# Optimization experiments

Measured on AMD Instinct MI355X. Metric: run time of the kernel, lower is better.

Reference implementation:

```python
import jax, jax.numpy as jnp
import numpy as np

EMB = 256  # embedding_dim


def setup_inputs() -> dict:
    key = jax.random.key(0)
    k1, k2, k3 = jax.random.split(key, 3)
    B, P, N, D = 32, 4, 1024, EMB
    x = jax.random.normal(k1, (B, P, N, D), dtype=jnp.float32)
    W_qkv = jax.random.normal(k2, (D, 1 + 2 * D), dtype=jnp.float32) * (1.0 / np.sqrt(D))
    b_qkv = jnp.zeros((1 + 2 * D,), dtype=jnp.float32)
    W_o = jax.random.normal(k3, (D, D), dtype=jnp.float32) * (1.0 / np.sqrt(D))
    b_o = jnp.zeros((D,), dtype=jnp.float32)
    return {"x": x, "W_qkv": W_qkv, "b_qkv": b_qkv, "W_o": W_o, "b_o": b_o}


def reference(x, W_qkv, b_qkv, W_o, b_o):
    # x: [B, P, N, D]
    D = W_o.shape[0]
    qkv = jnp.einsum('bpnd,de->bpne', x, W_qkv) + b_qkv  # [B,P,N,1+2D]
    q = qkv[..., :1]                 # [B,P,N,1]
    k = qkv[..., 1:1 + D]            # [B,P,N,D]
    v = jax.nn.relu(qkv[..., 1 + D:])  # [B,P,N,D]
    # softmax over the patch axis N (axis=2)
    context_scores = jax.nn.softmax(q, axis=2)  # [B,P,N,1]
    # dropout layers operate in inference mode here (identity)
    context_vector = jnp.sum(k * context_scores, axis=2, keepdims=True)  # [B,P,1,D]
    updated_values = v * context_vector  # broadcast multiply, [B,P,N,D]
    final = jnp.einsum('bpnd,de->bpne', updated_values, W_o) + b_o  # [B,P,N,D]
    return final
```

## Files before the change

### kernel.cpp

```cpp
#include <hip/hip_runtime.h>


typedef float  floatx4 __attribute__((ext_vector_type(4)));
typedef __bf16 bf16x8  __attribute__((ext_vector_type(8)));
typedef unsigned short u16;
typedef u16 u16x8 __attribute__((ext_vector_type(8)));

#define NGRP 128

__device__ __forceinline__ float bf2f(u16 u) {
    union { unsigned int i; float f; } c; c.i = ((unsigned int)u) << 16; return c.f;
}
__device__ __forceinline__ u16 f2bf(float f) {
    union { __bf16 h; u16 u; } c; c.h = (__bf16)f; return c.u;
}
__device__ __forceinline__ floatx4 mfma16(bf16x8 a, bf16x8 b, floatx4 c) {
    return __builtin_amdgcn_mfma_f32_16x16x32_bf16(a, b, c, 0, 0, 0);
}

__global__ __launch_bounds__(256) void k_prep(
    const float* __restrict__ Wqkv, const float* __restrict__ Wo,
    u16* __restrict__ Wvp, u16* __restrict__ Wop,
    float* __restrict__ wqp, float* __restrict__ y, float* __restrict__ Sg)
{
    const int i = blockIdx.x * 256 + threadIdx.x;
    const int j = i & 7, lane = (i >> 3) & 63, kk = (i >> 9) & 7, ct = i >> 12;
    const int k = kk * 32 + (lane >> 4) * 8 + j;
    Wvp[i] = f2bf(Wqkv[k * 513 + (257 + ct * 16 + (lane & 15))]);
    Wop[i] = f2bf(Wo[k * 256 + (ct * 16 + (lane & 15))]);
    if (i < 256) wqp[i] = Wqkv[i * 513];
    if (i < NGRP * 256) y[i] = 0.f;
    if (i < NGRP) Sg[i] = 0.f;
}

__global__ __launch_bounds__(256) void k_sum(
    const float* __restrict__ x, const float* __restrict__ wqp,
    const float* __restrict__ bqkv,
    float* __restrict__ y, float* __restrict__ Sg)
{
    const int tid = threadIdx.x;
    const int m0 = blockIdx.x * 64;
    const int g  = blockIdx.x >> 4;
    __shared__ float e_s[64];

    {
        const int r = tid >> 2, s = tid & 3;
        const float* xp = x + (size_t)(m0 + r) * 256 + s * 4;
        const float* wp = wqp + s * 4;
        float q = 0.f;
#pragma unroll
        for (int j = 0; j < 16; j++) {
            floatx4 xv = *(const floatx4*)(xp + j * 16);
            floatx4 wv = *(const floatx4*)(wp + j * 16);
            q += xv[0] * wv[0] + xv[1] * wv[1] + xv[2] * wv[2] + xv[3] * wv[3];
        }
        q += __shfl_xor(q, 1, 64);
        q += __shfl_xor(q, 2, 64);
        if (s == 0) e_s[r] = __expf(q + bqkv[0]);
    }
    __syncthreads();

    if (tid < 64) {
        float e = e_s[tid];
#pragma unroll
        for (int s = 32; s > 0; s >>= 1) e += __shfl_xor(e, s, 64);
        if (tid == 0) atomicAdd(Sg + g, e);
    }

    {
        float acc = 0.f;
        const float* xp = x + (size_t)m0 * 256 + tid;
#pragma unroll 8
        for (int r = 0; r < 64; r++) acc += e_s[r] * xp[r * 256];
        atomicAdd(y + g * 256 + tid, acc);
    }
}

__global__ __launch_bounds__(256) void k_cv(
    const float* __restrict__ Wqkv, const float* __restrict__ bqkv,
    const float* __restrict__ y, const float* __restrict__ Sg,
    float* __restrict__ cv)
{
    const int g = blockIdx.x, d = threadIdx.x;
    __shared__ float ys[256];
    ys[d] = y[g * 256 + d] * (1.0f / Sg[g]);
    __syncthreads();
    float acc = bqkv[1 + d];
    const float* wp = Wqkv + 1 + d;
#pragma unroll 4
    for (int t = 0; t < 256; t++) acc += ys[t] * wp[t * 513];
    cv[g * 256 + d] = acc;
}

__global__ __launch_bounds__(512, 4) void k_vo(
    const float* __restrict__ x, const u16* __restrict__ Wvp,
    const u16* __restrict__ Wop, const float* __restrict__ cv,
    const float* __restrict__ bqkv, const float* __restrict__ bo,
    float* __restrict__ out)
{
    const int tid = threadIdx.x;
    const int w = tid >> 6, lane = tid & 63, quad = lane >> 4, n16 = lane & 15;
    const int m0 = blockIdx.x * 64;
    const int g  = blockIdx.x >> 4;

    __shared__ u16 As[64 * 256];
    __shared__ float cvs[256];

    if (tid < 256) cvs[tid] = cv[g * 256 + tid];

#pragma unroll
    for (int it = 0; it < 4; it++) {
        const int c = it * 512 + tid;
        const int row = c >> 5, col = c & 31;
        const float* xp = x + (size_t)(m0 + row) * 256 + col * 8;
        floatx4 u0 = *(const floatx4*)xp;
        floatx4 u1 = *(const floatx4*)(xp + 4);
        u16x8 o;
        o[0] = f2bf(u0[0]); o[1] = f2bf(u0[1]); o[2] = f2bf(u0[2]); o[3] = f2bf(u0[3]);
        o[4] = f2bf(u1[0]); o[5] = f2bf(u1[1]); o[6] = f2bf(u1[2]); o[7] = f2bf(u1[3]);
        *(u16x8*)(As + row * 256 + ((col ^ (row & 15)) * 8)) = o;
    }
    __syncthreads();

    floatx4 acc[2][4];
#pragma unroll
    for (int i = 0; i < 2; i++)
#pragma unroll
        for (int rt = 0; rt < 4; rt++) acc[i][rt] = (floatx4){0.f, 0.f, 0.f, 0.f};

#pragma unroll
    for (int kk = 0; kk < 8; kk++) {
        bf16x8 a[4];
#pragma unroll
        for (int rt = 0; rt < 4; rt++) {
            const int row = rt * 16 + n16;
            a[rt] = __builtin_bit_cast(bf16x8,
                *(const u16x8*)(As + row * 256 + (((kk * 4 + quad) ^ n16) * 8)));
        }
#pragma unroll
        for (int i = 0; i < 2; i++) {
            const int ct = w + 8 * i;
            bf16x8 b = __builtin_bit_cast(bf16x8,
                *(const u16x8*)(Wvp + (size_t)((ct * 8 + kk) * 64 + lane) * 8));
#pragma unroll
            for (int rt = 0; rt < 4; rt++) acc[i][rt] = mfma16(a[rt], b, acc[i][rt]);
        }
    }
    __syncthreads();

#pragma unroll
    for (int i = 0; i < 2; i++) {
        const int col = (w + 8 * i) * 16 + n16;
        const float bias = bqkv[257 + col];
        const float scale = cvs[col];
        const int cc = col >> 3, co = col & 7;
#pragma unroll
        for (int rt = 0; rt < 4; rt++) {
#pragma unroll
            for (int r = 0; r < 4; r++) {
                const int row = rt * 16 + quad * 4 + r;
                const float vv = fmaxf(acc[i][rt][r] + bias, 0.f) * scale;
                As[row * 256 + ((cc ^ (row & 15)) * 8) + co] = f2bf(vv);
            }
        }
    }
    __syncthreads();

    floatx4 acc2[2][4];
#pragma unroll
    for (int i = 0; i < 2; i++)
#pragma unroll
        for (int rt = 0; rt < 4; rt++) acc2[i][rt] = (floatx4){0.f, 0.f, 0.f, 0.f};

#pragma unroll
    for (int kk = 0; kk < 8; kk++) {
        bf16x8 a[4];
#pragma unroll
        for (int rt = 0; rt < 4; rt++) {
            const int row = rt * 16 + n16;
            a[rt] = __builtin_bit_cast(bf16x8,
                *(const u16x8*)(As + row * 256 + (((kk * 4 + quad) ^ n16) * 8)));
        }
#pragma unroll
        for (int i = 0; i < 2; i++) {
            const int ct = w + 8 * i;
            bf16x8 b = __builtin_bit_cast(bf16x8,
                *(const u16x8*)(Wop + (size_t)((ct * 8 + kk) * 64 + lane) * 8));
#pragma unroll
            for (int rt = 0; rt < 4; rt++) acc2[i][rt] = mfma16(a[rt], b, acc2[i][rt]);
        }
    }

#pragma unroll
    for (int i = 0; i < 2; i++) {
        const int col = (w + 8 * i) * 16 + n16;
        const float bias = bo[col];
#pragma unroll
        for (int rt = 0; rt < 4; rt++) {
            const int rowb = m0 + rt * 16 + quad * 4;
#pragma unroll
            for (int r = 0; r < 4; r++)
                out[(size_t)(rowb + r) * 256 + col] = acc2[i][rt][r] + bias;
        }
    }
}

extern "C" void kernel_launch(void* const* d_in, const int* in_sizes, int n_in,
                              void* d_out, int out_size, void* d_ws, size_t ws_size,
                              hipStream_t stream)
{
    const float* x    = (const float*)d_in[0];
    const float* Wqkv = (const float*)d_in[1];
    const float* bqkv = (const float*)d_in[2];
    const float* Wo   = (const float*)d_in[3];
    const float* bo   = (const float*)d_in[4];
    float* out = (float*)d_out;

    char* ws = (char*)d_ws;
    u16*   Wvp = (u16*)(ws);
    u16*   Wop = (u16*)(ws + 131072);
    float* wqp = (float*)(ws + 262144);
    float* y   = (float*)(ws + 263168);
    float* Sg  = (float*)(ws + 394240);
    float* cv  = (float*)(ws + 394752);

    k_prep<<<256,  256, 0, stream>>>(Wqkv, Wo, Wvp, Wop, wqp, y, Sg);
    k_sum <<<2048, 256, 0, stream>>>(x, wqp, bqkv, y, Sg);
    k_cv  <<<NGRP, 256, 0, stream>>>(Wqkv, bqkv, y, Sg, cv);
    k_vo  <<<2048, 512, 0, stream>>>(x, Wvp, Wop, cv, bqkv, bo, out);
}
```

Baseline: 327.1 us.

## Cache bf16 x in k_sum, fuse cv into k_vo, double-buffer tiles via LDS DMA

```diff
diff --git a/kernel.cpp b/kernel.cpp
--- a/kernel.cpp
+++ b/kernel.cpp
@@ -16,6 +16,19 @@
 }
 __device__ __forceinline__ floatx4 mfma16(bf16x8 a, bf16x8 b, floatx4 c) {
     return __builtin_amdgcn_mfma_f32_16x16x32_bf16(a, b, c, 0, 0, 0);
+}
+
+__device__ __forceinline__ void bar_lgkm() {
+    __builtin_amdgcn_sched_barrier(0);
+    asm volatile("s_waitcnt lgkmcnt(0)" ::: "memory");
+    __builtin_amdgcn_s_barrier();
+    __builtin_amdgcn_sched_barrier(0);
+}
+
+__device__ __forceinline__ void dma16(const u16* src, u16* lds) {
+    __builtin_amdgcn_global_load_lds(
+        (const __attribute__((address_space(1))) unsigned int*)src,
+        (__attribute__((address_space(3))) unsigned int*)lds, 16, 0, 0);
 }
 
 __global__ __launch_bounds__(256) void k_prep(
@@ -36,7 +49,7 @@
 __global__ __launch_bounds__(256) void k_sum(
     const float* __restrict__ x, const float* __restrict__ wqp,
     const float* __restrict__ bqkv,
-    float* __restrict__ y, float* __restrict__ Sg)
+    float* __restrict__ y, float* __restrict__ Sg, u16* __restrict__ xb)
 {
     const int tid = threadIdx.x;
     const int m0 = blockIdx.x * 64;
@@ -57,6 +70,22 @@
         q += __shfl_xor(q, 1, 64);
         q += __shfl_xor(q, 2, 64);
         if (s == 0) e_s[r] = __expf(q + bqkv[0]);
+    }
+
+    {
+        u16* xt = xb + (size_t)blockIdx.x * 16384;
+#pragma unroll
+        for (int i = 0; i < 8; i++) {
+            const int chunk = i * 256 + tid;
+            const int row = chunk >> 5, col = chunk & 31;
+            const float* xp = x + (size_t)(m0 + row) * 256 + col * 8;
+            floatx4 u0 = *(const floatx4*)xp;
+            floatx4 u1 = *(const floatx4*)(xp + 4);
+            u16x8 o;
+            o[0] = f2bf(u0[0]); o[1] = f2bf(u0[1]); o[2] = f2bf(u0[2]); o[3] = f2bf(u0[3]);
+            o[4] = f2bf(u1[0]); o[5] = f2bf(u1[1]); o[6] = f2bf(u1[2]); o[7] = f2bf(u1[3]);
+            *(u16x8*)(xt + row * 256 + ((col ^ (row & 15)) * 8)) = o;
+        }
     }
     __syncthreads();
 
@@ -76,131 +105,144 @@
     }
 }
 
-__global__ __launch_bounds__(256) void k_cv(
-    const float* __restrict__ Wqkv, const float* __restrict__ bqkv,
-    const float* __restrict__ y, const float* __restrict__ Sg,
-    float* __restrict__ cv)
-{
-    const int g = blockIdx.x, d = threadIdx.x;
-    __shared__ float ys[256];
-    ys[d] = y[g * 256 + d] * (1.0f / Sg[g]);
-    __syncthreads();
-    float acc = bqkv[1 + d];
-    const float* wp = Wqkv + 1 + d;
-#pragma unroll 4
-    for (int t = 0; t < 256; t++) acc += ys[t] * wp[t * 513];
-    cv[g * 256 + d] = acc;
-}
-
 __global__ __launch_bounds__(512, 4) void k_vo(
-    const float* __restrict__ x, const u16* __restrict__ Wvp,
-    const u16* __restrict__ Wop, const float* __restrict__ cv,
+    const u16* __restrict__ xb, const u16* __restrict__ Wvp,
+    const u16* __restrict__ Wop, const float* __restrict__ y,
+    const float* __restrict__ Sg, const float* __restrict__ Wqkv,
     const float* __restrict__ bqkv, const float* __restrict__ bo,
     float* __restrict__ out)
 {
     const int tid = threadIdx.x;
     const int w = tid >> 6, lane = tid & 63, quad = lane >> 4, n16 = lane & 15;
-    const int m0 = blockIdx.x * 64;
-    const int g  = blockIdx.x >> 4;
-
-    __shared__ u16 As[64 * 256];
-    __shared__ float cvs[256];
-
-    if (tid < 256) cvs[tid] = cv[g * 256 + tid];
-
-#pragma unroll
-    for (int it = 0; it < 4; it++) {
-        const int c = it * 512 + tid;
-        const int row = c >> 5, col = c & 31;
-        const float* xp = x + (size_t)(m0 + row) * 256 + col * 8;
-        floatx4 u0 = *(const floatx4*)xp;
-        floatx4 u1 = *(const floatx4*)(xp + 4);
-        u16x8 o;
-        o[0] = f2bf(u0[0]); o[1] = f2bf(u0[1]); o[2] = f2bf(u0[2]); o[3] = f2bf(u0[3]);
-        o[4] = f2bf(u1[0]); o[5] = f2bf(u1[1]); o[6] = f2bf(u1[2]); o[7] = f2bf(u1[3]);
-        *(u16x8*)(As + row * 256 + ((col ^ (row & 15)) * 8)) = o;
+    const int b = blockIdx.x;
+    const int g = b >> 2;
+    const int tile0 = b * 4;
+
+    __shared__ u16 As[2][16384];
+    __shared__ float ys[256];
+    __shared__ float cvh[2][256];
+
+    {
+        const u16* src = xb + (size_t)tile0 * 16384;
+#pragma unroll
+        for (int i = 0; i < 4; i++)
+            dma16(src + (size_t)(i * 512 + tid) * 8, &As[0][(i * 512 + w * 64) * 8]);
+    }
+
+    const float rS = 1.0f / Sg[g];
+    if (tid < 256) ys[tid] = y[g * 256 + tid] * rS;
+    bar_lgkm();
+
+    {
+        const int d = tid & 255, half = tid >> 8;
+        float cvacc = (half == 0) ? bqkv[1 + d] : 0.f;
+        const float* wp = Wqkv + (size_t)(half * 128) * 513 + 1 + d;
+        const float* yp = ys + half * 128;
+#pragma unroll 4
+        for (int t = 0; t < 128; t++) cvacc += yp[t] * wp[(size_t)t * 513];
+        cvh[half][d] = cvacc;
     }
     __syncthreads();
 
-    floatx4 acc[2][4];
-#pragma unroll
-    for (int i = 0; i < 2; i++)
-#pragma unroll
-        for (int rt = 0; rt < 4; rt++) acc[i][rt] = (floatx4){0.f, 0.f, 0.f, 0.f};
-
-#pragma unroll
-    for (int kk = 0; kk < 8; kk++) {
-        bf16x8 a[4];
-#pragma unroll
-        for (int rt = 0; rt < 4; rt++) {
-            const int row = rt * 16 + n16;
-            a[rt] = __builtin_bit_cast(bf16x8,
-                *(const u16x8*)(As + row * 256 + (((kk * 4 + quad) ^ n16) * 8)));
-        }
-#pragma unroll
-        for (int i = 0; i < 2; i++) {
-            const int ct = w + 8 * i;
-            bf16x8 b = __builtin_bit_cast(bf16x8,
-                *(const u16x8*)(Wvp + (size_t)((ct * 8 + kk) * 64 + lane) * 8));
-#pragma unroll
-            for (int rt = 0; rt < 4; rt++) acc[i][rt] = mfma16(a[rt], b, acc[i][rt]);
-        }
-    }
-    __syncthreads();
-
+    float bvv[2], scv[2], bov[2];
 #pragma unroll
     for (int i = 0; i < 2; i++) {
         const int col = (w + 8 * i) * 16 + n16;
-        const float bias = bqkv[257 + col];
-        const float scale = cvs[col];
-        const int cc = col >> 3, co = col & 7;
-#pragma unroll
-        for (int rt = 0; rt < 4; rt++) {
-#pragma unroll
-            for (int r = 0; r < 4; r++) {
-                const int row = rt * 16 + quad * 4 + r;
-                const float vv = fmaxf(acc[i][rt][r] + bias, 0.f) * scale;
-                As[row * 256 + ((cc ^ (row & 15)) * 8) + co] = f2bf(vv);
-            }
-        }
-    }
-    __syncthreads();
-
-    floatx4 acc2[2][4];
-#pragma unroll
-    for (int i = 0; i < 2; i++)
-#pragma unroll
-        for (int rt = 0; rt < 4; rt++) acc2[i][rt] = (floatx4){0.f, 0.f, 0.f, 0.f};
-
-#pragma unroll
-    for (int kk = 0; kk < 8; kk++) {
-        bf16x8 a[4];
-#pragma unroll
-        for (int rt = 0; rt < 4; rt++) {
-            const int row = rt * 16 + n16;
-            a[rt] = __builtin_bit_cast(bf16x8,
-                *(const u16x8*)(As + row * 256 + (((kk * 4 + quad) ^ n16) * 8)));
-        }
+        bvv[i] = bqkv[257 + col];
+        scv[i] = cvh[0][col] + cvh[1][col];
+        bov[i] = bo[col];
+    }
+
+#pragma unroll
+    for (int it = 0; it < 4; ++it) {
+        const int cur = it & 1, nxt = cur ^ 1;
+        const int m0 = (tile0 + it) * 64;
+
+        if (it < 3) {
+            const u16* src = xb + (size_t)(tile0 + it + 1) * 16384;
+#pragma unroll
+            for (int i = 0; i < 4; i++)
+                dma16(src + (size_t)(i * 512 + tid) * 8,
+                      &As[nxt][(i * 512 + w * 64) * 8]);
+        }
+
+        floatx4 acc[2][4];
+#pragma unroll
+        for (int i = 0; i < 2; i++)
+#pragma unroll
+            for (int rt = 0; rt < 4; rt++) acc[i][rt] = (floatx4){0.f, 0.f, 0.f, 0.f};
+#pragma unroll
+        for (int kk = 0; kk < 8; kk++) {
+            bf16x8 a[4];
+#pragma unroll
+            for (int rt = 0; rt < 4; rt++) {
+                const int row = rt * 16 + n16;
+                a[rt] = __builtin_bit_cast(bf16x8,
+                    *(const u16x8*)(&As[cur][row * 256 + (((kk * 4 + quad) ^ n16) * 8)]));
+            }
+#pragma unroll
+            for (int i = 0; i < 2; i++) {
+                const int ct = w + 8 * i;
+                bf16x8 bfr = __builtin_bit_cast(bf16x8,
+                    *(const u16x8*)(Wvp + (size_t)((ct * 8 + kk) * 64 + lane) * 8));
+#pragma unroll
+                for (int rt = 0; rt < 4; rt++) acc[i][rt] = mfma16(a[rt], bfr, acc[i][rt]);
+            }
+        }
+        bar_lgkm();
+
 #pragma unroll
         for (int i = 0; i < 2; i++) {
-            const int ct = w + 8 * i;
-            bf16x8 b = __builtin_bit_cast(bf16x8,
-                *(const u16x8*)(Wop + (size_t)((ct * 8 + kk) * 64 + lane) * 8));
-#pragma unroll
-            for (int rt = 0; rt < 4; rt++) acc2[i][rt] = mfma16(a[rt], b, acc2[i][rt]);
-        }
-    }
-
-#pragma unroll
-    for (int i = 0; i < 2; i++) {
-        const int col = (w + 8 * i) * 16 + n16;
-        const float bias = bo[col];
-#pragma unroll
-        for (int rt = 0; rt < 4; rt++) {
-            const int rowb = m0 + rt * 16 + quad * 4;
-#pragma unroll
-            for (int r = 0; r < 4; r++)
-                out[(size_t)(rowb + r) * 256 + col] = acc2[i][rt][r] + bias;
+            const int col = (w + 8 * i) * 16 + n16;
+            const int cc = col >> 3, co = col & 7;
+#pragma unroll
+            for (int rt = 0; rt < 4; rt++) {
+#pragma unroll
+                for (int r = 0; r < 4; r++) {
+                    const int row = rt * 16 + quad * 4 + r;
+                    As[cur][row * 256 + ((cc ^ (row & 15)) * 8) + co] =
+                        f2bf(fmaxf(acc[i][rt][r] + bvv[i], 0.f) * scv[i]);
+                }
+            }
+        }
+        bar_lgkm();
+
+        floatx4 acc2[2][4];
+#pragma unroll
+        for (int i = 0; i < 2; i++)
+#pragma unroll
+            for (int rt = 0; rt < 4; rt++) acc2[i][rt] = (floatx4){0.f, 0.f, 0.f, 0.f};
+#pragma unroll
+        for (int kk = 0; kk < 8; kk++) {
+            bf16x8 a[4];
+#pragma unroll
+            for (int rt = 0; rt < 4; rt++) {
+                const int row = rt * 16 + n16;
+                a[rt] = __builtin_bit_cast(bf16x8,
+                    *(const u16x8*)(&As[cur][row * 256 + (((kk * 4 + quad) ^ n16) * 8)]));
+            }
+#pragma unroll
+            for (int i = 0; i < 2; i++) {
+                const int ct = w + 8 * i;
+                bf16x8 bfr = __builtin_bit_cast(bf16x8,
+                    *(const u16x8*)(Wop + (size_t)((ct * 8 + kk) * 64 + lane) * 8));
+#pragma unroll
+                for (int rt = 0; rt < 4; rt++) acc2[i][rt] = mfma16(a[rt], bfr, acc2[i][rt]);
+            }
+        }
+
+        __syncthreads();
+
+#pragma unroll
+        for (int i = 0; i < 2; i++) {
+            const int col = (w + 8 * i) * 16 + n16;
+#pragma unroll
+            for (int rt = 0; rt < 4; rt++) {
+                const int rowb = m0 + rt * 16 + quad * 4;
+#pragma unroll
+                for (int r = 0; r < 4; r++)
+                    out[(size_t)(rowb + r) * 256 + col] = acc2[i][rt][r] + bov[i];
+            }
         }
     }
 }
@@ -222,10 +264,9 @@
     float* wqp = (float*)(ws + 262144);
     float* y   = (float*)(ws + 263168);
     float* Sg  = (float*)(ws + 394240);
-    float* cv  = (float*)(ws + 394752);
+    u16*   xb  = (u16*)(ws + 394752);
 
     k_prep<<<256,  256, 0, stream>>>(Wqkv, Wo, Wvp, Wop, wqp, y, Sg);
-    k_sum <<<2048, 256, 0, stream>>>(x, wqp, bqkv, y, Sg);
-    k_cv  <<<NGRP, 256, 0, stream>>>(Wqkv, bqkv, y, Sg, cv);
-    k_vo  <<<2048, 512, 0, stream>>>(x, Wvp, Wop, cv, bqkv, bo, out);
-}
+    k_sum <<<2048, 256, 0, stream>>>(x, wqp, bqkv, y, Sg, xb);
+    k_vo  <<<512,  512, 0, stream>>>(xb, Wvp, Wop, y, Sg, Wqkv, bqkv, bo, out);
+}
```

New measurement: 320.4 us. -2.1%, faster.

## Stage bf16 copy of x in k_sum and DMA it into LDS in k_vo

Applied to the files above, without the earlier changes.

```diff
diff --git a/kernel.cpp b/kernel.cpp
--- a/kernel.cpp
+++ b/kernel.cpp
@@ -16,6 +16,12 @@
 }
 __device__ __forceinline__ floatx4 mfma16(bf16x8 a, bf16x8 b, floatx4 c) {
     return __builtin_amdgcn_mfma_f32_16x16x32_bf16(a, b, c, 0, 0, 0);
+}
+
+__device__ __forceinline__ void dma16(const u16* src, u16* lds) {
+    __builtin_amdgcn_global_load_lds(
+        (const __attribute__((address_space(1))) unsigned int*)src,
+        (__attribute__((address_space(3))) unsigned int*)lds, 16, 0, 0);
 }
 
 __global__ __launch_bounds__(256) void k_prep(
@@ -36,27 +42,63 @@
 __global__ __launch_bounds__(256) void k_sum(
     const float* __restrict__ x, const float* __restrict__ wqp,
     const float* __restrict__ bqkv,
-    float* __restrict__ y, float* __restrict__ Sg)
+    float* __restrict__ y, float* __restrict__ Sg, u16* __restrict__ xb)
 {
     const int tid = threadIdx.x;
     const int m0 = blockIdx.x * 64;
     const int g  = blockIdx.x >> 4;
+    const int cc = tid & 31, r0 = tid >> 5;
+    const int w = tid >> 6, lane = tid & 63;
     __shared__ float e_s[64];
-
-    {
-        const int r = tid >> 2, s = tid & 3;
-        const float* xp = x + (size_t)(m0 + r) * 256 + s * 4;
-        const float* wp = wqp + s * 4;
-        float q = 0.f;
-#pragma unroll
-        for (int j = 0; j < 16; j++) {
-            floatx4 xv = *(const floatx4*)(xp + j * 16);
-            floatx4 wv = *(const floatx4*)(wp + j * 16);
-            q += xv[0] * wv[0] + xv[1] * wv[1] + xv[2] * wv[2] + xv[3] * wv[3];
-        }
-        q += __shfl_xor(q, 1, 64);
-        q += __shfl_xor(q, 2, 64);
-        if (s == 0) e_s[r] = __expf(q + bqkv[0]);
+    __shared__ float ws4[4 * 256];
+
+    const floatx4 wq0 = *(const floatx4*)(wqp + cc * 8);
+    const floatx4 wq1 = *(const floatx4*)(wqp + cc * 8 + 4);
+    u16* xt = xb + (size_t)blockIdx.x * 16384;
+
+    float qp[8];
+    u16x8 o[8];
+#pragma unroll
+    for (int i = 0; i < 8; ++i) {
+        const int row = r0 + 8 * i;
+        const float* xp = x + (size_t)(m0 + row) * 256 + cc * 8;
+        floatx4 u0 = *(const floatx4*)xp;
+        floatx4 u1 = *(const floatx4*)(xp + 4);
+        qp[i] = u0[0] * wq0[0] + u0[1] * wq0[1] + u0[2] * wq0[2] + u0[3] * wq0[3]
+              + u1[0] * wq1[0] + u1[1] * wq1[1] + u1[2] * wq1[2] + u1[3] * wq1[3];
+        u16x8 t;
+        t[0] = f2bf(u0[0]); t[1] = f2bf(u0[1]); t[2] = f2bf(u0[2]); t[3] = f2bf(u0[3]);
+        t[4] = f2bf(u1[0]); t[5] = f2bf(u1[1]); t[6] = f2bf(u1[2]); t[7] = f2bf(u1[3]);
+        o[i] = t;
+        *(u16x8*)(xt + row * 256 + ((cc ^ (row & 15)) * 8)) = t;
+    }
+
+#pragma unroll
+    for (int m = 1; m <= 16; m <<= 1) {
+#pragma unroll
+        for (int i = 0; i < 8; ++i) qp[i] += __shfl_xor(qp[i], m, 64);
+    }
+    if ((tid & 31) == 0) {
+        const float bq0 = bqkv[0];
+#pragma unroll
+        for (int i = 0; i < 8; ++i) e_s[r0 + 8 * i] = __expf(qp[i] + bq0);
+    }
+    __syncthreads();
+
+    float yacc[8];
+#pragma unroll
+    for (int j = 0; j < 8; ++j) yacc[j] = 0.f;
+#pragma unroll
+    for (int i = 0; i < 8; ++i) {
+        const float e = e_s[r0 + 8 * i];
+#pragma unroll
+        for (int j = 0; j < 8; ++j) yacc[j] += e * bf2f(o[i][j]);
+    }
+#pragma unroll
+    for (int j = 0; j < 8; ++j) yacc[j] += __shfl_xor(yacc[j], 32, 64);
+    if (lane < 32) {
+#pragma unroll
+        for (int j = 0; j < 8; ++j) ws4[w * 256 + lane * 8 + j] = yacc[j];
     }
     __syncthreads();
 
@@ -66,13 +108,9 @@
         for (int s = 32; s > 0; s >>= 1) e += __shfl_xor(e, s, 64);
         if (tid == 0) atomicAdd(Sg + g, e);
     }
-
     {
-        float acc = 0.f;
-        const float* xp = x + (size_t)m0 * 256 + tid;
-#pragma unroll 8
-        for (int r = 0; r < 64; r++) acc += e_s[r] * xp[r * 256];
-        atomicAdd(y + g * 256 + tid, acc);
+        const float s = ws4[tid] + ws4[256 + tid] + ws4[512 + tid] + ws4[768 + tid];
+        atomicAdd(y + g * 256 + tid, s);
     }
 }
 
@@ -88,115 +126,108 @@
     float acc = bqkv[1 + d];
     const float* wp = Wqkv + 1 + d;
 #pragma unroll 4
-    for (int t = 0; t < 256; t++) acc += ys[t] * wp[t * 513];
+    for (int t = 0; t < 256; t++) acc += ys[t] * wp[(size_t)t * 513];
     cv[g * 256 + d] = acc;
 }
 
-__global__ __launch_bounds__(512, 4) void k_vo(
-    const float* __restrict__ x, const u16* __restrict__ Wvp,
+__global__ __launch_bounds__(256, 4) void k_vo(
+    const u16* __restrict__ xb, const u16* __restrict__ Wvp,
     const u16* __restrict__ Wop, const float* __restrict__ cv,
     const float* __restrict__ bqkv, const float* __restrict__ bo,
     float* __restrict__ out)
 {
     const int tid = threadIdx.x;
     const int w = tid >> 6, lane = tid & 63, quad = lane >> 4, n16 = lane & 15;
-    const int m0 = blockIdx.x * 64;
-    const int g  = blockIdx.x >> 4;
-
-    __shared__ u16 As[64 * 256];
+    const int m = blockIdx.x;
+    const int m0 = m * 32;
+    const int g  = m >> 5;
+
+    __shared__ u16 As[32 * 256];
     __shared__ float cvs[256];
 
-    if (tid < 256) cvs[tid] = cv[g * 256 + tid];
-
-#pragma unroll
-    for (int it = 0; it < 4; it++) {
-        const int c = it * 512 + tid;
-        const int row = c >> 5, col = c & 31;
-        const float* xp = x + (size_t)(m0 + row) * 256 + col * 8;
-        floatx4 u0 = *(const floatx4*)xp;
-        floatx4 u1 = *(const floatx4*)(xp + 4);
-        u16x8 o;
-        o[0] = f2bf(u0[0]); o[1] = f2bf(u0[1]); o[2] = f2bf(u0[2]); o[3] = f2bf(u0[3]);
-        o[4] = f2bf(u1[0]); o[5] = f2bf(u1[1]); o[6] = f2bf(u1[2]); o[7] = f2bf(u1[3]);
-        *(u16x8*)(As + row * 256 + ((col ^ (row & 15)) * 8)) = o;
-    }
-    __syncthreads();
-
-    floatx4 acc[2][4];
-#pragma unroll
-    for (int i = 0; i < 2; i++)
-#pragma unroll
-        for (int rt = 0; rt < 4; rt++) acc[i][rt] = (floatx4){0.f, 0.f, 0.f, 0.f};
-
+    cvs[tid] = cv[g * 256 + tid];
+
+    {
+        const u16* src = xb + (size_t)m * 8192;
+#pragma unroll
+        for (int it = 0; it < 4; ++it)
+            dma16(src + (size_t)(it * 256 + tid) * 8, &As[(it * 256 + w * 64) * 8]);
+    }
+    __syncthreads();
+
+    floatx4 acc[4][2];
+#pragma unroll
+    for (int i = 0; i < 4; i++)
+#pragma unroll
+        for (int rt = 0; rt < 2; rt++) acc[i][rt] = (floatx4){0.f, 0.f, 0.f, 0.f};
 #pragma unroll
     for (int kk = 0; kk < 8; kk++) {
-        bf16x8 a[4];
-#pragma unroll
-        for (int rt = 0; rt < 4; rt++) {
+        bf16x8 a[2];
+#pragma unroll
+        for (int rt = 0; rt < 2; rt++) {
             const int row = rt * 16 + n16;
             a[rt] = __builtin_bit_cast(bf16x8,
-                *(const u16x8*)(As + row * 256 + (((kk * 4 + quad) ^ n16) * 8)));
-        }
-#pragma unroll
-        for (int i = 0; i < 2; i++) {
-            const int ct = w + 8 * i;
-            bf16x8 b = __builtin_bit_cast(bf16x8,
+                *(const u16x8*)(&As[row * 256 + (((kk * 4 + quad) ^ n16) * 8)]));
+        }
+#pragma unroll
+        for (int i = 0; i < 4; i++) {
+            const int ct = w + 4 * i;
+            bf16x8 bfr = __builtin_bit_cast(bf16x8,
                 *(const u16x8*)(Wvp + (size_t)((ct * 8 + kk) * 64 + lane) * 8));
 #pragma unroll
-            for (int rt = 0; rt < 4; rt++) acc[i][rt] = mfma16(a[rt], b, acc[i][rt]);
-        }
-    }
-    __syncthreads();
-
-#pragma unroll
-    for (int i = 0; i < 2; i++) {
-        const int col = (w + 8 * i) * 16 + n16;
+            for (int rt = 0; rt < 2; rt++) acc[i][rt] = mfma16(a[rt], bfr, acc[i][rt]);
+        }
+    }
+    __syncthreads();
+
+#pragma unroll
+    for (int i = 0; i < 4; i++) {
+        const int col = (w + 4 * i) * 16 + n16;
         const float bias = bqkv[257 + col];
         const float scale = cvs[col];
-        const int cc = col >> 3, co = col & 7;
-#pragma unroll
-        for (int rt = 0; rt < 4; rt++) {
+        const int cchunk = col >> 3, co = col & 7;
+#pragma unroll
+        for (int rt = 0; rt < 2; rt++) {
 #pragma unroll
             for (int r = 0; r < 4; r++) {
                 const int row = rt * 16 + quad * 4 + r;
-                const float vv = fmaxf(acc[i][rt][r] + bias, 0.f) * scale;
-                As[row * 256 + ((cc ^ (row & 15)) * 8) + co] = f2bf(vv);
+                As[row * 256 + ((cchunk ^ (row & 15)) * 8) + co] =
+                    f2bf(fmaxf(acc[i][rt][r] + bias, 0.f) * scale);
             }
         }
     }
     __syncthreads();
 
-    floatx4 acc2[2][4];
-#pragma unroll
-    for (int i = 0; i < 2; i++)
-#pragma unroll
-        for (int rt = 0; rt < 4; rt++) acc2[i][rt] = (floatx4){0.f, 0.f, 0.f, 0.f};
-
+    floatx4 acc2[4][2];
+#pragma unroll
+    for (int i = 0; i < 4; i++)
+#pragma unroll
+        for (int rt = 0; rt < 2; rt++) acc2[i][rt] = (floatx4){0.f, 0.f, 0.f, 0.f};
 #pragma unroll
     for (int kk = 0; kk < 8; kk++) {
-        bf16x8 a[4];
-#pragma unroll
-        for (int rt = 0; rt < 4; rt++) {
+        bf16x8 a[2];
+#pragma unroll
+        for (int rt = 0; rt < 2; rt++) {
             const int row = rt * 16 + n16;
             a[rt] = __builtin_bit_cast(bf16x8,
-                *(const u16x8*)(As + row * 256 + (((kk * 4 + quad) ^ n16) * 8)));
-        }
-#pragma unroll
-        for (int i = 0; i < 2; i++) {
-            const int ct = w + 8 * i;
-            bf16x8 b = __builtin_bit_cast(bf16x8,
+                *(const u16x8*)(&As[row * 256 + (((kk * 4 + quad) ^ n16) * 8)]));
+        }
+#pragma unroll
+        for (int i = 0; i < 4; i++) {
+            const int ct = w + 4 * i;
+            bf16x8 bfr = __builtin_bit_cast(bf16x8,
                 *(const u16x8*)(Wop + (size_t)((ct * 8 + kk) * 64 + lane) * 8));
 #pragma unroll
-            for (int rt = 0; rt < 4; rt++) acc2[i][rt] = mfma16(a[rt], b, acc2[i][rt]);
-        }
-    }
-
-#pragma unroll
-    for (int i = 0; i < 2; i++) {
-        const int col = (w + 8 * i) * 16 + n16;
+            for (int rt = 0; rt < 2; rt++) acc2[i][rt] = mfma16(a[rt], bfr, acc2[i][rt]);
+        }
+    }
+
+#pragma unroll
+    for (int i = 0; i < 4; i++) {
+        const int col = (w + 4 * i) * 16 + n16;
         const float bias = bo[col];
 #pragma unroll
-        for (int rt = 0; rt < 4; rt++) {
+        for (int rt = 0; rt < 2; rt++) {
             const int rowb = m0 + rt * 16 + quad * 4;
 #pragma unroll
             for (int r = 0; r < 4; r++)
@@ -223,9 +254,10 @@
     float* y   = (float*)(ws + 263168);
     float* Sg  = (float*)(ws + 394240);
     float* cv  = (float*)(ws + 394752);
+    u16*   xb  = (u16*)(ws + 525824);
 
     k_prep<<<256,  256, 0, stream>>>(Wqkv, Wo, Wvp, Wop, wqp, y, Sg);
-    k_sum <<<2048, 256, 0, stream>>>(x, wqp, bqkv, y, Sg);
+    k_sum <<<2048, 256, 0, stream>>>(x, wqp, bqkv, y, Sg, xb);
     k_cv  <<<NGRP, 256, 0, stream>>>(Wqkv, bqkv, y, Sg, cv);
-    k_vo  <<<2048, 512, 0, stream>>>(x, Wvp, Wop, cv, bqkv, bo, out);
-}
+    k_vo  <<<4096, 256, 0, stream>>>(xb, Wvp, Wop, cv, bqkv, bo, out);
+}
```

Measured after the change: 328.0 us. No clear change (+0.2%).
